# Kernel optimization log

Measured on AMD Instinct MI355X. Metric: run time of the kernel, lower is better.

Reference implementation:

```python
import jax, jax.numpy as jnp
import numpy as np

B, T, N, K, d = 8, 12, 325, 8, 64
D = K * d


def setup_inputs() -> dict:
    key = jax.random.key(0)
    ks = jax.random.split(key, 12)
    s = 0.02
    f32 = jnp.float32
    inp = {
        "X": jax.random.normal(ks[0], (B, T, N, D), f32),
        "STE": jax.random.normal(ks[1], (B, T, N, D), f32),
        "Wq": (jax.random.normal(ks[2], (2 * D, D), f32) * s),
        "bq": jnp.zeros((D,), f32),
        "Wk": (jax.random.normal(ks[3], (2 * D, D), f32) * s),
        "bk": jnp.zeros((D,), f32),
        "Wv": (jax.random.normal(ks[4], (2 * D, D), f32) * s),
        "bv": jnp.zeros((D,), f32),
        "W1": (jax.random.normal(ks[5], (D, D), f32) * s),
        "b1": jnp.zeros((D,), f32),
        "W2": (jax.random.normal(ks[6], (D, D), f32) * s),
        "b2": jnp.zeros((D,), f32),
        "attn_mask": 0,
    }
    return inp


def reference(X, STE, Wq, bq, Wk, bk, Wv, bv, W1, b1, W2, b2, attn_mask):
    # X, STE: [B, T, N, D]
    Xc = jnp.concatenate([X, STE], axis=-1)          # [B,T,N,2D]
    q = jax.nn.relu(Xc @ Wq + bq).reshape(B, T, N, K, d)
    k = jax.nn.relu(Xc @ Wk + bk).reshape(B, T, N, K, d)
    v = jax.nn.relu(Xc @ Wv + bv).reshape(B, T, N, K, d)

    # scores: [B, K, T, N, N] (attention over spatial/node axis N)
    scores = jnp.einsum('btnhe,btmhe->bhtnm', q, k)
    # mask_flag=False -> TriangularCausalMask applied (upper-tri masked with -inf)
    causal = jnp.triu(jnp.ones((N, N), dtype=bool), 1)
    scores = jnp.where(causal, -jnp.inf, scores)
    # original scales AFTER masking; -inf / sqrt(d) stays -inf
    scores = scores / jnp.sqrt(jnp.asarray(d, scores.dtype))
    attn = jax.nn.softmax(scores, axis=-1)
    # dropout: eval mode (identity)

    ctx = jnp.einsum('bhtnm,btmhe->btnhe', attn, v).reshape(B, T, N, D)
    out = jax.nn.relu(ctx @ W1 + b1) @ W2 + b2        # [B,T,N,D]

    # match torch's head-major cat(dim=0): [K*B, T, N, N]
    attn_full = jnp.transpose(attn, (1, 0, 2, 3, 4)).reshape(K * B, T, N, N)
    return out, attn_full
```

## Files before the change

kernel.cpp:

```cpp
#include <hip/hip_runtime.h>
#include <hip/hip_bf16.h>

typedef __hip_bfloat16 bf16;
using f32x4  = __attribute__((ext_vector_type(4))) float;
using short8 = __attribute__((ext_vector_type(8))) short;

#define M_ROWS   31200
#define M_PAD    31232
#define N_TOK    325
#define D_MODEL  512
#define QKV_LD   1536

#define GLOBAL_AS(p) ((const __attribute__((address_space(1))) unsigned int*)(p))
#define LDS_AS(p)    ((__attribute__((address_space(3))) unsigned int*)(p))

__global__ void init_flag(int* flag) { if (threadIdx.x == 0) *flag = 0; }

__global__ void detect_dtype(const unsigned short* __restrict__ x, int* flag)
{
    int i = blockIdx.x * 256 + threadIdx.x;
    unsigned short h = x[i];
    int e = (h >> 7) & 0xFF;
    if (e >= 135) atomicOr(flag, 1);
}

__device__ __forceinline__ float load_in(const void* p, size_t i, bool f32)
{
    return f32 ? ((const float*)p)[i] : __bfloat162float(((const bf16*)p)[i]);
}

__global__ void concat_cast(const void* __restrict__ X, const void* __restrict__ STE,
                            bf16* __restrict__ Xc, const int* __restrict__ flag)
{
    const bool f32 = (*flag != 0);
    int idx = blockIdx.x * 256 + threadIdx.x;
    int r = idx >> 7, c8 = (idx & 127) << 3;
    short8 v = {0, 0, 0, 0, 0, 0, 0, 0};
    if (r < M_ROWS) {
        const void* src = (c8 < 512) ? X : STE;
        int cc = c8 & 511;
        if (f32) {
            const float* s = (const float*)src + (size_t)r * 512 + cc;
            float4 a = *(const float4*)s;
            float4 b = *(const float4*)(s + 4);
            ((bf16*)&v)[0] = __float2bfloat16(a.x); ((bf16*)&v)[1] = __float2bfloat16(a.y);
            ((bf16*)&v)[2] = __float2bfloat16(a.z); ((bf16*)&v)[3] = __float2bfloat16(a.w);
            ((bf16*)&v)[4] = __float2bfloat16(b.x); ((bf16*)&v)[5] = __float2bfloat16(b.y);
            ((bf16*)&v)[6] = __float2bfloat16(b.z); ((bf16*)&v)[7] = __float2bfloat16(b.w);
        } else {
            v = *(const short8*)((const bf16*)src + (size_t)r * 512 + cc);
        }
    }
    *(short8*)&Xc[(size_t)r * 1024 + c8] = v;
}

__global__ void transpose_w_all(
    const void* __restrict__ Wq, const void* __restrict__ Wk,
    const void* __restrict__ Wv, const void* __restrict__ W1,
    const void* __restrict__ W2, bf16* __restrict__ BtQKV,
    bf16* __restrict__ W1T, bf16* __restrict__ W2T,
    const int* __restrict__ flag)
{
    __shared__ float tile[32][33];
    const bool f32 = (*flag != 0);
    const int bid = blockIdx.x;
    const void* src;
    bf16* dst;
    int krows, tile_id;
    if (bid < 1536) {
        const int wsel = bid / 512;
        tile_id = bid % 512;
        src = (wsel == 0) ? Wq : ((wsel == 1) ? Wk : Wv);
        dst = BtQKV + (size_t)wsel * 512 * 1024;
        krows = 1024;
    } else {
        const int wsel = (bid - 1536) / 256;
        tile_id = (bid - 1536) % 256;
        src = (wsel == 0) ? W1 : W2;
        dst = (wsel == 0) ? W1T : W2T;
        krows = 512;
    }
    const int ncols = 512;
    const int nt = (tile_id % 16) * 32;
    const int kt = (tile_id / 16) * 32;
    const int tx = threadIdx.x & 31, ty = threadIdx.x >> 5;
#pragma unroll
    for (int r = 0; r < 32; r += 8)
        tile[ty + r][tx] = load_in(src, (size_t)(kt + ty + r) * ncols + (nt + tx), f32);
    __syncthreads();
#pragma unroll
    for (int r = 0; r < 32; r += 8)
        dst[(size_t)(nt + ty + r) * krows + (kt + tx)] = __float2bfloat16(tile[tx][ty + r]);
}

__global__ void prep_bias(const void* __restrict__ bq, const void* __restrict__ bk,
                          const void* __restrict__ bv, const void* __restrict__ b1,
                          const void* __restrict__ b2,
                          float* __restrict__ biasQKV, float* __restrict__ b1f,
                          float* __restrict__ b2f, const int* __restrict__ flag)
{
    const bool f32 = (*flag != 0);
    int i = blockIdx.x * 256 + threadIdx.x;
    if (i < 512) {
        biasQKV[i]        = load_in(bq, i, f32);
        biasQKV[512 + i]  = load_in(bk, i, f32);
        biasQKV[1024 + i] = load_in(bv, i, f32);
        b1f[i] = load_in(b1, i, f32);
        b2f[i] = load_in(b2, i, f32);
    }
}

template<int OUTF32, int RELU>
__global__ __launch_bounds__(512) void gemm_lds256(
    const bf16* __restrict__ A, int lda,
    const bf16* __restrict__ Bt, int ldb,
    const float* __restrict__ bias, void* __restrict__ Cv,
    int Mvalid, int Kdim, int ldc, int nby)
{
    __shared__ alignas(16) bf16 As0[256 * 32];
    __shared__ alignas(16) bf16 As1[256 * 32];
    __shared__ alignas(16) bf16 Bs0[128 * 32];
    __shared__ alignas(16) bf16 Bs1[128 * 32];
    const int cpx = gridDim.x >> 3;
    const int swz = (blockIdx.x & 7) * cpx + (blockIdx.x >> 3);
    const int m0 = (swz / nby) * 256;
    const int n0 = (swz % nby) * 128;
    const int t = threadIdx.x, wave = t >> 6, lane = t & 63;
    const int wm = (wave >> 1) * 64, wn = (wave & 1) * 64;
    const int lrow = lane & 15, lk8 = (lane >> 4) * 8;
    const int srow = lane >> 2, scol = (lane & 3) << 3;
    f32x4 acc[4][4] = {};
    const int nk = Kdim >> 6;

    for (int ks = 0; ks < nk; ++ks) {
        const int kk = ks << 6;
        __syncthreads();
#pragma unroll
        for (int c = 0; c < 2; ++c) {
            const int arow = wave * 32 + c * 16;
            const bf16* ga = A + (size_t)(m0 + arow + srow) * lda + kk + scol;
            __builtin_amdgcn_global_load_lds(GLOBAL_AS(ga),      LDS_AS(As0 + arow * 32), 16, 0, 0);
            __builtin_amdgcn_global_load_lds(GLOBAL_AS(ga + 32), LDS_AS(As1 + arow * 32), 16, 0, 0);
        }
        {
            const int brow = wave * 16;
            const bf16* gb = Bt + (size_t)(n0 + brow + srow) * ldb + kk + scol;
            __builtin_amdgcn_global_load_lds(GLOBAL_AS(gb),      LDS_AS(Bs0 + brow * 32), 16, 0, 0);
            __builtin_amdgcn_global_load_lds(GLOBAL_AS(gb + 32), LDS_AS(Bs1 + brow * 32), 16, 0, 0);
        }
        __syncthreads();
        short8 af[4], bfr[4];
#pragma unroll
        for (int i = 0; i < 4; ++i) {
            af[i]  = *(const short8*)&As0[(wm + i * 16 + lrow) * 32 + lk8];
            bfr[i] = *(const short8*)&Bs0[(wn + i * 16 + lrow) * 32 + lk8];
        }
#pragma unroll
        for (int i = 0; i < 4; ++i)
#pragma unroll
            for (int j = 0; j < 4; ++j)
                acc[i][j] = __builtin_amdgcn_mfma_f32_16x16x32_bf16(
                    af[i], bfr[j], acc[i][j], 0, 0, 0);
#pragma unroll
        for (int i = 0; i < 4; ++i) {
            af[i]  = *(const short8*)&As1[(wm + i * 16 + lrow) * 32 + lk8];
            bfr[i] = *(const short8*)&Bs1[(wn + i * 16 + lrow) * 32 + lk8];
        }
#pragma unroll
        for (int i = 0; i < 4; ++i)
#pragma unroll
            for (int j = 0; j < 4; ++j)
                acc[i][j] = __builtin_amdgcn_mfma_f32_16x16x32_bf16(
                    af[i], bfr[j], acc[i][j], 0, 0, 0);
    }

    const int r4 = (lane >> 4) * 4;
#pragma unroll
    for (int i = 0; i < 4; ++i) {
#pragma unroll
        for (int r = 0; r < 4; ++r) {
            int grow = m0 + wm + i * 16 + r4 + r;
            if (OUTF32 && grow >= Mvalid) continue;
#pragma unroll
            for (int j = 0; j < 4; ++j) {
                int gcol = n0 + wn + j * 16 + lrow;
                float v  = acc[i][j][r] + bias[gcol];
                if (RELU) v = fmaxf(v, 0.0f);
                if (OUTF32)
                    ((float*)Cv)[(size_t)grow * ldc + gcol] = v;
                else
                    ((bf16*)Cv)[(size_t)grow * ldc + gcol] = __float2bfloat16(v);
            }
        }
    }
}

#define KS_LD  72
#define VT_LD  354

__device__ __forceinline__ int tile_of(int w, int it)
{
    const int m[3][8] = {
        {20, 19, 18, 17, 16, 15, 14, 13},
        { 5,  6,  7,  8,  9, 10, 11, 12},
        {-1, -1, -1,  1,  2,  3,  4,  0},
    };
    return m[it][w];
}

__global__ __launch_bounds__(512) void attn_kernel(
    bf16* __restrict__ qkv, float* __restrict__ attn_out)
{
    __shared__ alignas(16) bf16 Ks[336 * KS_LD];
    __shared__ alignas(16) bf16 Vt[64 * VT_LD + 32];
    __shared__ alignas(16) bf16 ptile[8][16 * 40];
    const int t = threadIdx.x, lane = t & 63, w = t >> 6;
    const int h = blockIdx.x & 7, bt = blockIdx.x >> 3;
    const size_t rowbase = (size_t)bt * N_TOK;
    const int lrow = lane & 15, lk8 = (lane >> 4) * 8;
    const int r4 = (lane >> 4) * 4;
    const int b = bt / 12, tt2 = bt % 12;
    const size_t hb_base = (((size_t)(h * 8 + b)) * 12 + tt2) * N_TOK;

    for (int task = t; task < 336 * 8; task += 512) {
        int m = task >> 3, e0 = (task & 7) << 3;
        short8 v = {0, 0, 0, 0, 0, 0, 0, 0};
        if (m < N_TOK)
            v = *(const short8*)(qkv + (rowbase + m) * QKV_LD + 512 + h * 64 + e0);
        *(short8*)&Ks[m * KS_LD + e0] = v;
    }
    for (int task = t; task < 352 * 8; task += 512) {
        int m = task >> 3, e0 = (task & 7) << 3;
        short8 v = {0, 0, 0, 0, 0, 0, 0, 0};
        if (m < N_TOK)
            v = *(const short8*)(qkv + (rowbase + m) * QKV_LD + 1024 + h * 64 + e0);
#pragma unroll
        for (int j = 0; j < 8; ++j)
            Vt[(e0 + j) * VT_LD + m] = ((bf16*)&v)[j];
    }
    __syncthreads();

    for (int it = 0; it < 3; ++it) {
        const int tile = tile_of(w, it);
        if (tile < 0) continue;
        const int r0 = tile * 16;

        int qrow = r0 + lrow; if (qrow > N_TOK - 1) qrow = N_TOK - 1;
        const bf16* qp = qkv + (rowbase + qrow) * QKV_LD + h * 64 + lk8;
        short8 qa0 = *(const short8*)(qp);
        short8 qa1 = *(const short8*)(qp + 32);

        f32x4 f[22];
        f[21] = (f32x4){0.f, 0.f, 0.f, 0.f};
#pragma unroll
        for (int ct = 0; ct < 21; ++ct) {
            if (ct <= tile) {
                f32x4 a = {0.f, 0.f, 0.f, 0.f};
                short8 kb0 = *(const short8*)&Ks[(ct * 16 + lrow) * KS_LD + lk8];
                short8 kb1 = *(const short8*)&Ks[(ct * 16 + lrow) * KS_LD + 32 + lk8];
                __builtin_amdgcn_s_setprio(1);
                a = __builtin_amdgcn_mfma_f32_16x16x32_bf16(qa0, kb0, a, 0, 0, 0);
                a = __builtin_amdgcn_mfma_f32_16x16x32_bf16(qa1, kb1, a, 0, 0, 0);
                __builtin_amdgcn_s_setprio(0);
                f[ct] = a;
            }
        }

        float mx[4] = {-1e30f, -1e30f, -1e30f, -1e30f};
        float sm[4] = {0.f, 0.f, 0.f, 0.f};
#pragma unroll
        for (int ct = 0; ct < 21; ++ct) {
            if (ct <= tile) {
                const int c = ct * 16 + lrow;
#pragma unroll
                for (int r = 0; r < 4; ++r)
                    if (c <= r0 + r4 + r) mx[r] = fmaxf(mx[r], f[ct][r]);
            }
        }
#pragma unroll
        for (int r = 0; r < 4; ++r) {
#pragma unroll
            for (int o = 1; o < 16; o <<= 1) mx[r] = fmaxf(mx[r], __shfl_xor(mx[r], o));
        }
#pragma unroll
        for (int ct = 0; ct < 21; ++ct) {
            if (ct <= tile) {
                const int c = ct * 16 + lrow;
#pragma unroll
                for (int r = 0; r < 4; ++r) {
                    float e = (c <= r0 + r4 + r)
                                  ? __expf((f[ct][r] - mx[r]) * 0.125f) : 0.f;
                    f[ct][r] = e;
                    sm[r] += e;
                }
            }
        }
#pragma unroll
        for (int r = 0; r < 4; ++r) {
#pragma unroll
            for (int o = 1; o < 16; o <<= 1) sm[r] += __shfl_xor(sm[r], o);
            sm[r] = 1.0f / sm[r];
        }
#pragma unroll
        for (int ct = 0; ct < 21; ++ct) {
            if (ct <= tile) {
#pragma unroll
                for (int r = 0; r < 4; ++r) f[ct][r] *= sm[r];
            }
        }

#pragma unroll
        for (int ct = 0; ct < 21; ++ct) {
            const int c = ct * 16 + lrow;
            if (c < N_TOK) {
#pragma unroll
                for (int r = 0; r < 4; ++r) {
                    const int n = r0 + r4 + r;
                    if (n < N_TOK) {
                        float v = (ct <= tile && c <= n) ? f[ct][r] : 0.f;
                        attn_out[(hb_base + n) * N_TOK + c] = v;
                    }
                }
            }
        }

        f32x4 acc[4] = {};
        bf16* pt = &ptile[w][0];
#pragma unroll
        for (int s = 0; s < 11; ++s) {
            if (s <= (tile >> 1)) {
#pragma unroll
                for (int half = 0; half < 2; ++half) {
                    const int ct2 = 2 * s + half;
                    const int c = ct2 * 16 + lrow;
#pragma unroll
                    for (int r = 0; r < 4; ++r) {
                        const int n = r0 + r4 + r;
                        float v = (ct2 <= tile && c <= n) ? f[ct2][r] : 0.f;
                        pt[(r4 + r) * 40 + half * 16 + lrow] = __float2bfloat16(v);
                    }
                }
                short8 aa = *(const short8*)&pt[lrow * 40 + lk8];
                __builtin_amdgcn_s_setprio(1);
#pragma unroll
                for (int e = 0; e < 4; ++e) {
                    short8 bb = *(const short8*)&Vt[(e * 16 + lrow) * VT_LD + s * 32 + lk8];
                    acc[e] = __builtin_amdgcn_mfma_f32_16x16x32_bf16(aa, bb, acc[e], 0, 0, 0);
                }
                __builtin_amdgcn_s_setprio(0);
            }
        }

#pragma unroll
        for (int e = 0; e < 4; ++e) {
#pragma unroll
            for (int r = 0; r < 4; ++r) {
                const int n = r0 + r4 + r;
                if (n < N_TOK)
                    qkv[(rowbase + n) * QKV_LD + h * 64 + e * 16 + lrow] =
                        __float2bfloat16(acc[e][r]);
            }
        }
    }
}

extern "C" void kernel_launch(void* const* d_in, const int* in_sizes, int n_in,
                              void* d_out, int out_size, void* d_ws, size_t ws_size,
                              hipStream_t stream)
{
    const void* X   = d_in[0];
    const void* STE = d_in[1];
    const void* Wq  = d_in[2];
    const void* bq  = d_in[3];
    const void* Wk  = d_in[4];
    const void* bk  = d_in[5];
    const void* Wv  = d_in[6];
    const void* bv  = d_in[7];
    const void* W1  = d_in[8];
    const void* b1  = d_in[9];
    const void* W2  = d_in[10];
    const void* b2  = d_in[11];

    float* out0     = (float*)d_out;
    float* attn_out = (float*)d_out + (size_t)M_ROWS * D_MODEL;
    bf16*  Xc       = (bf16*)attn_out;

    char* ws = (char*)d_ws;
    bf16*  qkv   = (bf16*)(ws);
    bf16*  BtQKV = (bf16*)(ws + 95944704);
    bf16*  W1T   = (bf16*)(ws + 99090432);
    bf16*  W2T   = (bf16*)(ws + 99614720);
    float* biasQ = (float*)(ws + 100139008);
    float* b1f   = (float*)(ws + 100145152);
    float* b2f   = (float*)(ws + 100147200);
    int*   flag  = (int*)(ws + 100149248);
    bf16*  hbuf  = qkv + 512;

    init_flag<<<1, 64, 0, stream>>>(flag);
    detect_dtype<<<64, 256, 0, stream>>>((const unsigned short*)X, flag);

    transpose_w_all<<<2048, 256, 0, stream>>>(Wq, Wk, Wv, W1, W2,
                                              BtQKV, W1T, W2T, flag);
    prep_bias<<<2, 256, 0, stream>>>(bq, bk, bv, b1, b2, biasQ, b1f, b2f, flag);

    concat_cast<<<(M_PAD * 128) / 256, 256, 0, stream>>>(X, STE, Xc, flag);

    gemm_lds256<0, 1><<<122 * 12, 512, 0, stream>>>(
        Xc, 1024, BtQKV, 1024, biasQ, qkv, M_PAD, 1024, QKV_LD, 12);

    attn_kernel<<<768, 512, 0, stream>>>(qkv, attn_out);

    gemm_lds256<0, 1><<<122 * 4, 512, 0, stream>>>(
        qkv, QKV_LD, W1T, 512, b1f, hbuf, M_PAD, 512, QKV_LD, 4);

    gemm_lds256<1, 0><<<122 * 4, 512, 0, stream>>>(
        hbuf, QKV_LD, W2T, 512, b2f, out0, M_ROWS, 512, D_MODEL, 4);
}
```

Measured before the change: 358.5 us.

## Drop K shared-memory staging, recompute QK scores, store unnormalized probs as bf16

Removes the K tile from LDS and reads K rows directly from global memory. QK^T is now computed twice, once for the row max and once for exp/sum, so the float score tiles no longer have to stay in registers. Unnormalized probabilities are packed as bf16 and normalization is deferred to the attention output and PV result. launch_bounds is raised to allow 4 blocks per CU. The intent is lower LDS and register pressure for higher occupancy, at the cost of doubled QK MFMAs, repeated global K loads, and attention weights now rounded through bf16 before being written in fp32.

Result: slower. 474.1 us (+32.2%).

```diff
diff --git a/kernel.cpp b/kernel.cpp
--- a/kernel.cpp
+++ b/kernel.cpp
@@ -4,6 +4,7 @@
 typedef __hip_bfloat16 bf16;
 using f32x4  = __attribute__((ext_vector_type(4))) float;
 using short8 = __attribute__((ext_vector_type(8))) short;
+using short4v = __attribute__((ext_vector_type(4))) short;
 
 #define M_ROWS   31200
 #define M_PAD    31232
@@ -195,7 +196,6 @@
     }
 }
 
-#define KS_LD  72
 #define VT_LD  354
 
 __device__ __forceinline__ int tile_of(int w, int it)
@@ -208,10 +208,9 @@
     return m[it][w];
 }
 
-__global__ __launch_bounds__(512) void attn_kernel(
+__global__ __launch_bounds__(512, 4) void attn_kernel(
     bf16* __restrict__ qkv, float* __restrict__ attn_out)
 {
-    __shared__ alignas(16) bf16 Ks[336 * KS_LD];
     __shared__ alignas(16) bf16 Vt[64 * VT_LD + 32];
     __shared__ alignas(16) bf16 ptile[8][16 * 40];
     const int t = threadIdx.x, lane = t & 63, w = t >> 6;
@@ -221,14 +220,8 @@
     const int r4 = (lane >> 4) * 4;
     const int b = bt / 12, tt2 = bt % 12;
     const size_t hb_base = (((size_t)(h * 8 + b)) * 12 + tt2) * N_TOK;
-
-    for (int task = t; task < 336 * 8; task += 512) {
-        int m = task >> 3, e0 = (task & 7) << 3;
-        short8 v = {0, 0, 0, 0, 0, 0, 0, 0};
-        if (m < N_TOK)
-            v = *(const short8*)(qkv + (rowbase + m) * QKV_LD + 512 + h * 64 + e0);
-        *(short8*)&Ks[m * KS_LD + e0] = v;
-    }
+    const bf16* kbase = qkv + rowbase * QKV_LD + 512 + h * 64;
+
     for (int task = t; task < 352 * 8; task += 512) {
         int m = task >> 3, e0 = (task & 7) << 3;
         short8 v = {0, 0, 0, 0, 0, 0, 0, 0};
@@ -250,63 +243,59 @@
         short8 qa0 = *(const short8*)(qp);
         short8 qa1 = *(const short8*)(qp + 32);
 
-        f32x4 f[22];
-        f[21] = (f32x4){0.f, 0.f, 0.f, 0.f};
+        float mx[4] = {-1e30f, -1e30f, -1e30f, -1e30f};
 #pragma unroll
         for (int ct = 0; ct < 21; ++ct) {
             if (ct <= tile) {
+                const bf16* kr = kbase + (size_t)(ct * 16 + lrow) * QKV_LD;
+                short8 kb0 = *(const short8*)(kr + lk8);
+                short8 kb1 = *(const short8*)(kr + 32 + lk8);
                 f32x4 a = {0.f, 0.f, 0.f, 0.f};
-                short8 kb0 = *(const short8*)&Ks[(ct * 16 + lrow) * KS_LD + lk8];
-                short8 kb1 = *(const short8*)&Ks[(ct * 16 + lrow) * KS_LD + 32 + lk8];
                 __builtin_amdgcn_s_setprio(1);
                 a = __builtin_amdgcn_mfma_f32_16x16x32_bf16(qa0, kb0, a, 0, 0, 0);
                 a = __builtin_amdgcn_mfma_f32_16x16x32_bf16(qa1, kb1, a, 0, 0, 0);
                 __builtin_amdgcn_s_setprio(0);
-                f[ct] = a;
-            }
-        }
-
-        float mx[4] = {-1e30f, -1e30f, -1e30f, -1e30f};
+                const int c = ct * 16 + lrow;
+#pragma unroll
+                for (int r = 0; r < 4; ++r)
+                    if (c <= r0 + r4 + r) mx[r] = fmaxf(mx[r], a[r]);
+            }
+        }
+#pragma unroll
+        for (int r = 0; r < 4; ++r) {
+#pragma unroll
+            for (int o = 1; o < 16; o <<= 1) mx[r] = fmaxf(mx[r], __shfl_xor(mx[r], o));
+        }
+
         float sm[4] = {0.f, 0.f, 0.f, 0.f};
+        short4v pb[22] = {};
 #pragma unroll
         for (int ct = 0; ct < 21; ++ct) {
             if (ct <= tile) {
-                const int c = ct * 16 + lrow;
-#pragma unroll
-                for (int r = 0; r < 4; ++r)
-                    if (c <= r0 + r4 + r) mx[r] = fmaxf(mx[r], f[ct][r]);
-            }
-        }
-#pragma unroll
-        for (int r = 0; r < 4; ++r) {
-#pragma unroll
-            for (int o = 1; o < 16; o <<= 1) mx[r] = fmaxf(mx[r], __shfl_xor(mx[r], o));
-        }
-#pragma unroll
-        for (int ct = 0; ct < 21; ++ct) {
-            if (ct <= tile) {
+                const bf16* kr = kbase + (size_t)(ct * 16 + lrow) * QKV_LD;
+                short8 kb0 = *(const short8*)(kr + lk8);
+                short8 kb1 = *(const short8*)(kr + 32 + lk8);
+                f32x4 a = {0.f, 0.f, 0.f, 0.f};
+                __builtin_amdgcn_s_setprio(1);
+                a = __builtin_amdgcn_mfma_f32_16x16x32_bf16(qa0, kb0, a, 0, 0, 0);
+                a = __builtin_amdgcn_mfma_f32_16x16x32_bf16(qa1, kb1, a, 0, 0, 0);
+                __builtin_amdgcn_s_setprio(0);
                 const int c = ct * 16 + lrow;
 #pragma unroll
                 for (int r = 0; r < 4; ++r) {
                     float e = (c <= r0 + r4 + r)
-                                  ? __expf((f[ct][r] - mx[r]) * 0.125f) : 0.f;
-                    f[ct][r] = e;
+                                  ? __expf((a[r] - mx[r]) * 0.125f) : 0.f;
                     sm[r] += e;
+                    ((bf16*)&pb[ct])[r] = __float2bfloat16(e);
                 }
             }
         }
+        float inv[4];
 #pragma unroll
         for (int r = 0; r < 4; ++r) {
 #pragma unroll
             for (int o = 1; o < 16; o <<= 1) sm[r] += __shfl_xor(sm[r], o);
-            sm[r] = 1.0f / sm[r];
-        }
-#pragma unroll
-        for (int ct = 0; ct < 21; ++ct) {
-            if (ct <= tile) {
-#pragma unroll
-                for (int r = 0; r < 4; ++r) f[ct][r] *= sm[r];
-            }
+            inv[r] = 1.0f / sm[r];
         }
 
 #pragma unroll
@@ -317,7 +306,8 @@
                 for (int r = 0; r < 4; ++r) {
                     const int n = r0 + r4 + r;
                     if (n < N_TOK) {
-                        float v = (ct <= tile && c <= n) ? f[ct][r] : 0.f;
+                        float v = (ct <= tile)
+                            ? __bfloat162float(((bf16*)&pb[ct])[r]) * inv[r] : 0.f;
                         attn_out[(hb_base + n) * N_TOK + c] = v;
                     }
                 }
@@ -332,12 +322,11 @@
 #pragma unroll
                 for (int half = 0; half < 2; ++half) {
                     const int ct2 = 2 * s + half;
-                    const int c = ct2 * 16 + lrow;
 #pragma unroll
                     for (int r = 0; r < 4; ++r) {
-                        const int n = r0 + r4 + r;
-                        float v = (ct2 <= tile && c <= n) ? f[ct2][r] : 0.f;
-                        pt[(r4 + r) * 40 + half * 16 + lrow] = __float2bfloat16(v);
+                        bf16 v = (ct2 <= tile) ? ((bf16*)&pb[ct2])[r]
+                                               : __float2bfloat16(0.f);
+                        pt[(r4 + r) * 40 + half * 16 + lrow] = v;
                     }
                 }
                 short8 aa = *(const short8*)&pt[lrow * 40 + lk8];
@@ -358,7 +347,7 @@
                 const int n = r0 + r4 + r;
                 if (n < N_TOK)
                     qkv[(rowbase + n) * QKV_LD + h * 64 + e * 16 + lrow] =
-                        __float2bfloat16(acc[e][r]);
+                        __float2bfloat16(acc[e][r] * inv[r]);
             }
         }
     }
```
